# Optimization experiments

Hardware: AMD Instinct MI355X
Metric: run time of the kernel (lower is better)

## Reference

```python
import jax, jax.numpy as jnp
import numpy as np
from jax import lax

G = 64      # ngroup
CPN = 4     # channels per group in hidden layers
H, W = 32, 64
K = 5       # conv kernel
BIN = 8     # bin_num
BIAS = 3.5  # (bin_num-1)/2
NMIX = 3    # GMM components (batch replicas)
SCALE = 65536.0


def _group_mask(cout, cin, strict):
    # wavefront causality: tap (dg, di, dj) allowed iff dg+di+dj < 0 (strict) or <= 0
    g = jnp.arange(G)
    dg = g[None, :] - g[:, None]                      # (Gout, Gin)
    off = jnp.arange(K) - K // 2
    dd = off[:, None] + off[None, :]                  # (K, K)
    tot = dg[:, :, None, None] + dd[None, None, :, :]
    m = (tot < 0) if strict else (tot <= 0)
    m = jnp.repeat(jnp.repeat(m, cout, axis=0), cin, axis=1)
    return m.astype(jnp.float32)                      # (G*cout, G*cin, K, K)


def _cconv(x, w, b, m, relu):
    y = lax.conv_general_dilated(x, w * m, (1, 1), 'SAME',
                                 dimension_numbers=('NCHW', 'OIHW', 'NCHW'))
    y = y + b[None, :, None, None]
    return jax.nn.relu(y) if relu else y


def setup_inputs() -> dict:
    key = jax.random.key(0)
    ks = jax.random.split(key, 8)
    data = jax.random.randint(ks[0], (1, G, H, W), 0, BIN).astype(jnp.float32)
    mask = jax.random.randint(ks[1], (1, G, H, W), 0, 2).astype(jnp.float32)
    s = 0.05
    w_in = jax.random.normal(ks[2], (G * CPN, G, K, K), jnp.float32) * s
    b_in = jnp.zeros((G * CPN,), jnp.float32)
    w_hid = jax.random.normal(ks[3], (10, G * CPN, G * CPN, K, K), jnp.float32) * s
    b_hid = jnp.zeros((10, G * CPN), jnp.float32)
    w_out = jax.random.normal(ks[4], (G * NMIX, G * CPN, K, K), jnp.float32) * s
    b_out = jnp.zeros((G * NMIX,), jnp.float32)
    return dict(data=data, mask=mask, w_in=w_in, b_in=b_in,
                w_hid=w_hid, b_hid=b_hid, w_out=w_out, b_out=b_out)


def reference(data, mask, w_in, b_in, w_hid, b_hid, w_out, b_out):
    m_in = _group_mask(CPN, 1, True)      # first layer: strict (excludes current group)
    m_hid = _group_mask(CPN, CPN, False)
    m_out = _group_mask(NMIX, CPN, False)
    tdata = (data - BIAS) * mask
    x = jnp.concatenate([tdata, tdata, tdata], axis=0)   # (3, G, H, W)
    x = _cconv(x, w_in, b_in, m_in, True)
    for i in range(5):                                   # 5 residual blocks
        h = _cconv(x, w_hid[2 * i], b_hid[2 * i], m_hid, True)
        h = _cconv(h, w_hid[2 * i + 1], b_hid[2 * i + 1], m_hid, True)
        x = x + h
    y = _cconv(x, w_out, b_out, m_out, False)            # (3, G*3, H, W)
    y = y.reshape(NMIX, G, NMIX, H, W)                   # batch replica m -> mixture m
    logits = y[:, :, 0]
    mu = y[:, :, 1]
    sig = jax.nn.softplus(y[:, :, 2]) + 1e-6
    wts = jax.nn.softmax(logits, axis=0)                 # (3, G, H, W)
    edges = jnp.arange(BIN, dtype=jnp.float32) + 0.5 - BIAS
    z = (edges[:, None, None, None, None] - mu[None]) / (sig[None] * jnp.float32(np.sqrt(2.0)))
    cdf = 0.5 * (1.0 + lax.erf(z))                       # (BIN, 3, G, H, W)
    table = jnp.einsum('kmghw,mghw->ghwk', cdf, wts) * SCALE
    return table                                         # (G, H, W, BIN) quantizable CDF
```

## Files before the change

kernel.cpp:

```cpp
#include <hip/hip_runtime.h>
#include <math.h>

typedef _Float16 f16;
typedef _Float16 f16x8 __attribute__((ext_vector_type(8)));
typedef float f32x4 __attribute__((ext_vector_type(4)));

#define HH 32
#define WW 64
#define NPX 2048
#define SLOTS 68
#define CHS 78336
#define LOSCALE 2048.0f
#define INV_LOSCALE 4.8828125e-4f

typedef const __attribute__((address_space(1))) void gvoid;
typedef __attribute__((address_space(3))) void lvoid;
__device__ __forceinline__ void gload_lds16(const void* g, void* l) {
    __builtin_amdgcn_global_load_lds((gvoid*)g, (lvoid*)l, 16, 0, 0);
}

__device__ __forceinline__ void repack_tile(
    const float* __restrict__ W, f16* __restrict__ WP, float* RAWF,
    int Cin, int nCoT, int nCic, int cpg_in_log2, int limb, int is_out,
    int coT, int cic, int plane)
{
    const int nt = blockDim.x, t = threadIdx.x;
    const int co0 = coT * 16, ci0 = cic * 32;
    for (int u = t; u < 3200; u += nt) {
        int co16 = u / 200, j4 = u - co16 * 200;
        int co_p = co0 + co16;
        int co_orig = is_out ? 3 * (co_p >> 1) + 1 + (co_p & 1) : co_p;
        float4 v = *(const float4*)(W + (size_t)(co_orig * Cin + ci0) * 25 + j4 * 4);
        *(float4*)&RAWF[co16 * 800 + j4 * 4] = v;
    }
    __syncthreads();
    const int base = (coT * nCic + cic) * 512;
    const int tapStride = nCoT * nCic * 512;
    for (int e = t; e < 12800; e += nt) {
        int tap = e >> 9, r = e & 511;
        int co16 = r >> 5, ci32 = r & 31;
        int ky = tap / 5, kx = tap - 5 * ky;
        int co_p = co0 + co16;
        int g_out = is_out ? (co_p >> 1) : (co_p >> 2);
        int g_in = (ci0 + ci32) >> cpg_in_log2;
        float v = 0.f;
        if (ky + kx <= limb + g_out - g_in)
            v = RAWF[co16 * 800 + ci32 * 25 + tap];
        f16 vh = (f16)v;
        int dst = base + tap * tapStride + co16 * 32 + ci32;
        WP[dst] = vh;
        WP[plane + dst] = (f16)((v - (float)vh) * LOSCALE);
    }
}

__global__ __launch_bounds__(256) void init_kernel(
    const float* __restrict__ data, const float* __restrict__ mask,
    f16* __restrict__ PQ, f16* __restrict__ X0,
    const float* __restrict__ w_in, f16* __restrict__ WP)
{
    __shared__ __align__(16) float RAWF[12800];
    const int b = blockIdx.x, t = threadIdx.x;
    if (b < 1224) {
        *(int4*)(PQ + (size_t)(b * 256 + t) * 8) = make_int4(0, 0, 0, 0);
    } else if (b < 1836) {
        int e = (b - 1224) * 256 + t;
        int si = e >> 6, ci = e & 63;
        int row = si / 68, slot = si - row * 68;
        float v = 0.f;
        if (row >= 2 && row < 34 && slot >= 2 && slot < 66) {
            int px = (row - 2) * 64 + (slot - 2);
            v = (data[ci * NPX + px] - 3.5f) * mask[ci * NPX + px];
        }
        int dst = (ci >> 5) * CHS + si * 32 + (ci & 31);
        X0[dst] = (f16)v;
        X0[156672 + dst] = (f16)0.f;
    } else {
        int rb = b - 1836;
        repack_tile(w_in, WP, RAWF, 64, 16, 2, 0, 3, 0, rb >> 1, rb & 1, 409600);
    }
}

__global__ __launch_bounds__(320, 3) void conv_kernel(
    const f16* __restrict__ IN, int Cin, int inPlane,
    const f16* __restrict__ WP, int wPlane,
    const float* __restrict__ bias,
    const f16* __restrict__ RES, int resPlane,
    f16* __restrict__ OA, int oaPlane,
    float* __restrict__ OT,
    int nmt, int Coutp, int cpg_out, int cpg_in, int limb, int mode,
    const float* __restrict__ rW, f16* __restrict__ rWP,
    int rCin, int rnCoT, int rnCic, int rcpg_in_log2, int rlimb, int ris_out,
    int rplane, int nConv)
{
    __shared__ __align__(16) char SMEM[51200];
    f16* BL = (f16*)SMEM;
    float* RED = (float*)SMEM;

    if (blockIdx.x >= (unsigned)nConv) {
        int rb = blockIdx.x - nConv;
        repack_tile(rW, rWP, (float*)SMEM, rCin, rnCoT, rnCic,
                    rcpg_in_log2, rlimb, ris_out, rb / rnCic, rb % rnCic, rplane);
        return;
    }

    const int t = threadIdx.x;
    const int kw = t >> 6;
    const int lane = t & 63, l15 = lane & 15, q = lane >> 4;

    const int b = blockIdx.x;
    const int p3 = b & 7, r = b >> 3;
    int pairIdx, slot, h_;
    if (nmt == 16) { pairIdx = p3;     h_ = r & 31; slot = r >> 5; }
    else           { pairIdx = p3 & 3; h_ = r;      slot = p3 >> 2; }
    const int h = h_;
    const int mt = slot ? (nmt - 1 - pairIdx) : pairIdx;
    const int co0 = mt * 16;
    const int g_max = (co0 + 15) / cpg_out;

    int cnt[5];
#pragma unroll
    for (int kx = 0; kx < 5; kx++) {
        int c = (g_max + limb - (kw + kx) + 1) * cpg_in;
        c = c < Cin ? c : Cin;
        cnt[kx] = c > 0 ? c : 0;
    }
    int ci_top = (g_max + limb + 1) * cpg_in;
    ci_top = ci_top < Cin ? ci_top : Cin;

    const f16* src[9];
#pragma unroll
    for (int rr = 0; rr < 9; rr++) {
        int u = rr * 320 + t;
        if (u >= 2720) u = 0;
        int pl = u >= 1360 ? 1 : 0;
        int rem = u - pl * 1360;
        src[rr] = IN + (size_t)pl * inPlane + h * 2176 + rem * 8;
    }

    f32x4 acc_h[4], acc_m[4];
#pragma unroll
    for (int j = 0; j < 4; j++) {
        acc_h[j] = (f32x4){0.f, 0.f, 0.f, 0.f};
        acc_m[j] = (f32x4){0.f, 0.f, 0.f, 0.f};
    }

    const size_t kxs = (size_t)Coutp * Cin;
    const f16* wb0 = WP + (size_t)(kw * 5 * (Coutp >> 4) + mt) * ((size_t)Cin << 4)
                   + l15 * 32 + q * 8;

    int coff = 0;
    for (int ci0 = 0; ci0 < ci_top; ci0 += 32, coff += CHS) {
        __syncthreads();
#pragma unroll
        for (int rr = 0; rr < 9; rr++) {
            int ub = rr * 320 + kw * 64;
            if (ub < 2720)
                gload_lds16(src[rr] + coff, BL + ub * 8);
        }
        const f16* wb = wb0 + (ci0 >> 5) * 512;
        f16x8 cah, cal, nah, nal;
        if (ci0 < cnt[0]) {
            cah = *(const f16x8*)(wb);
            cal = *(const f16x8*)(wb + wPlane);
        }
        __syncthreads();

#pragma unroll
        for (int kx = 0; kx < 5; kx++) {
            if (ci0 >= cnt[kx]) break;
            if (kx < 4 && ci0 < cnt[kx + 1]) {
                nah = *(const f16x8*)(wb + (kx + 1) * kxs);
                nal = *(const f16x8*)(wb + (kx + 1) * kxs + wPlane);
            }
            f16x8 bh[4], bl[4];
#pragma unroll
            for (int j = 0; j < 4; j++) {
                int slt = j * 16 + l15 + kx;
                bh[j] = *(const f16x8*)&BL[(0 * 5 + kw) * (SLOTS * 32) + slt * 32 + q * 8];
                bl[j] = *(const f16x8*)&BL[(1 * 5 + kw) * (SLOTS * 32) + slt * 32 + q * 8];
            }
#pragma unroll
            for (int j = 0; j < 4; j++) {
                acc_h[j] = __builtin_amdgcn_mfma_f32_16x16x32_f16(cah, bh[j], acc_h[j], 0, 0, 0);
                acc_m[j] = __builtin_amdgcn_mfma_f32_16x16x32_f16(cah, bl[j], acc_m[j], 0, 0, 0);
                acc_m[j] = __builtin_amdgcn_mfma_f32_16x16x32_f16(cal, bh[j], acc_m[j], 0, 0, 0);
            }
            cah = nah; cal = nal;
        }
    }

    __syncthreads();
#pragma unroll
    for (int j = 0; j < 4; j++) {
        f32x4 v;
#pragma unroll
        for (int rr = 0; rr < 4; rr++)
            v[rr] = acc_h[j][rr] + acc_m[j][rr] * INV_LOSCALE;
        *(f32x4*)&RED[(kw * 64 + j * 16 + l15) * 20 + q * 4] = v;
    }
    __syncthreads();

    if (mode == 0) {
        for (int c = t; c < 1024; c += 320) {
            int px = c >> 4, col = c & 15;
            float v = bias[co0 + col];
#pragma unroll
            for (int k5 = 0; k5 < 5; k5++) v += RED[(k5 * 64 + px) * 20 + col];
            v = fmaxf(v, 0.f);
            int cc = co0 + col;
            int o = (cc >> 5) * CHS + ((h + 2) * SLOTS + px + 2) * 32 + (cc & 31);
            if (RES) v += (float)RES[o] + (float)RES[resPlane + o] * INV_LOSCALE;
            f16 vh = (f16)v;
            OA[o] = vh;
            OA[oaPlane + o] = (f16)((v - (float)vh) * LOSCALE);
        }
    } else {
        for (int c = t; c < 1024; c += 320) {
            int px = c >> 4, col = c & 15;
            float v = bias[3 * ((co0 + col) >> 1) + 1 + (col & 1)];
#pragma unroll
            for (int k5 = 0; k5 < 5; k5++) v += RED[(k5 * 64 + px) * 20 + col];
            RED[px * 20 + col] = v;
        }
        __syncthreads();
        for (int c = t; c < 512; c += 320) {
            int px = c >> 3, gl = c & 7;
            float mu = RED[px * 20 + 2 * gl];
            float s  = RED[px * 20 + 2 * gl + 1];
            float sp = fmaxf(s, 0.f) + log1pf(expf(-fabsf(s)));
            float sig = sp + 1e-6f;
            float inv = 1.f / (sig * 1.41421356237f);
            int g = (co0 >> 1) + gl;
            float* o = OT + ((size_t)g * NPX + h * WW + px) * 8;
#pragma unroll
            for (int k = 0; k < 8; k++) {
                float z = ((float)k - 3.0f - mu) * inv;
                o[k] = 32768.f * (1.f + erff(z));
            }
        }
    }
}

extern "C" void kernel_launch(void* const* d_in, const int* in_sizes, int n_in,
                              void* d_out, int out_size, void* d_ws, size_t ws_size,
                              hipStream_t stream) {
    const float* data  = (const float*)d_in[0];
    const float* mask  = (const float*)d_in[1];
    const float* w_in  = (const float*)d_in[2];
    const float* b_in  = (const float*)d_in[3];
    const float* w_hid = (const float*)d_in[4];
    const float* b_hid = (const float*)d_in[5];
    const float* w_out = (const float*)d_in[6];
    const float* b_out = (const float*)d_in[7];
    float* out = (float*)d_out;

    f16* WPA = (f16*)d_ws;
    f16* WPB = WPA + 3276800;
    f16* P   = WPB + 3276800;
    f16* Q   = P + 1253376;
    f16* X0  = Q + 1253376;

    init_kernel<<<1868, 256, 0, stream>>>(data, mask, P, X0, w_in, WPA);

    f16* cur = WPA;
    f16* nxt = WPB;

    conv_kernel<<<640, 320, 0, stream>>>(X0, 64, 156672, cur, 409600,
        b_in, nullptr, 0, P, 626688, nullptr, 16, 256, 4, 1, 3, 0,
        w_hid, nxt, 256, 16, 8, 2, 4, 0, 1638400, 512);
    { f16* tmp = cur; cur = nxt; nxt = tmp; }

    for (int k = 1; k <= 10; ++k) {
        const int isLast = (k == 10);
        const float* rw = isLast ? w_out : (w_hid + (size_t)k * 1638400);
        const int rgrid = isLast ? 64 : 128;
        const int rnCoT = isLast ? 8 : 16;
        const int ris   = isLast ? 1 : 0;
        const int rpl   = isLast ? 819200 : 1638400;
        if (k & 1)
            conv_kernel<<<512 + rgrid, 320, 0, stream>>>(P, 256, 626688, cur, 1638400,
                b_hid + (size_t)(k - 1) * 256, nullptr, 0, Q, 626688, nullptr,
                16, 256, 4, 4, 4, 0,
                rw, nxt, 256, rnCoT, 8, 2, 4, ris, rpl, 512);
        else
            conv_kernel<<<512 + rgrid, 320, 0, stream>>>(Q, 256, 626688, cur, 1638400,
                b_hid + (size_t)(k - 1) * 256, P, 626688, P, 626688, nullptr,
                16, 256, 4, 4, 4, 0,
                rw, nxt, 256, rnCoT, 8, 2, 4, ris, rpl, 512);
        f16* tmp = cur; cur = nxt; nxt = tmp;
    }

    conv_kernel<<<256, 320, 0, stream>>>(P, 256, 626688, cur, 819200,
        b_out, nullptr, 0, nullptr, 0, out, 8, 128, 2, 4, 4, 1,
        nullptr, nullptr, 256, 8, 1, 2, 4, 0, 0, 256);
}
```

Measured before the change: 450.5 us.

## Give each wave a private LDS input region and drop block-wide barriers

Each wave (kw) now loads only the input row it needs into its own LDS region via global_load_lds, rather than the whole block cooperatively loading a shared buffer. This removes the two __syncthreads per channel chunk and uses per-wave vmcnt/lgkmcnt waits instead, so the next chunk's load can be issued right after the current chunk's LDS reads. The cost is some redundant global traffic and more LDS footprint. Correctness relies on the per-wave regions not overlapping and on the wait counters covering the async LDS writes.

```diff
diff --git a/kernel.cpp b/kernel.cpp
--- a/kernel.cpp
+++ b/kernel.cpp
@@ -126,16 +126,19 @@
     }
     int ci_top = (g_max + limb + 1) * cpg_in;
     ci_top = ci_top < Cin ? ci_top : Cin;
-
-    const f16* src[9];
-#pragma unroll
-    for (int rr = 0; rr < 9; rr++) {
-        int u = rr * 320 + t;
-        if (u >= 2720) u = 0;
-        int pl = u >= 1360 ? 1 : 0;
-        int rem = u - pl * 1360;
-        src[rr] = IN + (size_t)pl * inPlane + h * 2176 + rem * 8;
-    }
+    const int NT = (ci_top + 31) >> 5;
+
+    int soff[9];
+    const int rowg = (h + kw) * 2176;
+#pragma unroll
+    for (int r9 = 0; r9 < 9; ++r9) {
+        int u = r9 * 64 + lane;
+        if (u > 543) u = 543;
+        int pl = u >= 272 ? 1 : 0;
+        int rem = u - (pl ? 272 : 0);
+        soff[r9] = pl * inPlane + rowg + rem * 8;
+    }
+    f16* const wreg = BL + kw * 4608;
 
     f32x4 acc_h[4], acc_m[4];
 #pragma unroll
@@ -148,23 +151,22 @@
     const f16* wb0 = WP + (size_t)(kw * 5 * (Coutp >> 4) + mt) * ((size_t)Cin << 4)
                    + l15 * 32 + q * 8;
 
-    int coff = 0;
-    for (int ci0 = 0; ci0 < ci_top; ci0 += 32, coff += CHS) {
-        __syncthreads();
-#pragma unroll
-        for (int rr = 0; rr < 9; rr++) {
-            int ub = rr * 320 + kw * 64;
-            if (ub < 2720)
-                gload_lds16(src[rr] + coff, BL + ub * 8);
-        }
-        const f16* wb = wb0 + (ci0 >> 5) * 512;
+#pragma unroll
+    for (int r9 = 0; r9 < 9; ++r9)
+        gload_lds16(IN + soff[r9], wreg + r9 * 512);
+
+    for (int it = 0; it < NT; ++it) {
+        const int ci0 = it << 5;
+        const f16* wb = wb0 + it * 512;
         f16x8 cah, cal, nah, nal;
         if (ci0 < cnt[0]) {
             cah = *(const f16x8*)(wb);
             cal = *(const f16x8*)(wb + wPlane);
         }
-        __syncthreads();
-
+        asm volatile("s_waitcnt vmcnt(0)" ::: "memory");
+
+        const f16* bhp = wreg + q * 8;
+        const f16* blp = bhp + 2176;
 #pragma unroll
         for (int kx = 0; kx < 5; kx++) {
             if (ci0 >= cnt[kx]) break;
@@ -176,8 +178,8 @@
 #pragma unroll
             for (int j = 0; j < 4; j++) {
                 int slt = j * 16 + l15 + kx;
-                bh[j] = *(const f16x8*)&BL[(0 * 5 + kw) * (SLOTS * 32) + slt * 32 + q * 8];
-                bl[j] = *(const f16x8*)&BL[(1 * 5 + kw) * (SLOTS * 32) + slt * 32 + q * 8];
+                bh[j] = *(const f16x8*)(bhp + slt * 32);
+                bl[j] = *(const f16x8*)(blp + slt * 32);
             }
 #pragma unroll
             for (int j = 0; j < 4; j++) {
@@ -186,6 +188,13 @@
                 acc_m[j] = __builtin_amdgcn_mfma_f32_16x16x32_f16(cal, bh[j], acc_m[j], 0, 0, 0);
             }
             cah = nah; cal = nal;
+        }
+        if (it + 1 < NT) {
+            asm volatile("s_waitcnt lgkmcnt(0)" ::: "memory");
+            const int coff = (it + 1) * CHS;
+#pragma unroll
+            for (int r9 = 0; r9 < 9; ++r9)
+                gload_lds16(IN + soff[r9] + coff, wreg + r9 * 512);
         }
     }
 
```

Result: faster. 424.5 us (-5.8%).
